# Performance work log

Hardware: AMD Instinct MI355X
Metric: run time of the kernel (lower is better)

## Reference

```python
import jax, jax.numpy as jnp
import numpy as np

B, IN_CH, OUT_CH = 4, 64, 128
N_HIGH, N_LOW = 163842, 40962
GROUPS, EPS, SLOPE = 4, 1e-5, 0.2


def setup_inputs() -> dict:
    key = jax.random.key(0)
    ks = jax.random.split(key, 6)
    x = jax.random.normal(ks[0], (B, IN_CH, N_HIGH), jnp.float32)
    pool_neigh = jax.random.randint(ks[1], (N_LOW * 7,), 0, N_HIGH, dtype=jnp.int32)
    conv_neigh = jax.random.randint(ks[2], (N_LOW * 7,), 0, N_LOW, dtype=jnp.int32)
    W1 = jax.random.normal(ks[3], (OUT_CH, 7 * IN_CH), jnp.float32) / np.float32(np.sqrt(7 * IN_CH))
    b1 = jnp.zeros((OUT_CH,), jnp.float32)
    W2 = jax.random.normal(ks[4], (OUT_CH, 7 * OUT_CH), jnp.float32) / np.float32(np.sqrt(7 * OUT_CH))
    b2 = jnp.zeros((OUT_CH,), jnp.float32)
    return dict(x=x, pool_neigh=pool_neigh, conv_neigh=conv_neigh,
                W1=W1, b1=b1, gn1_w=jnp.ones((OUT_CH,), jnp.float32), gn1_b=jnp.zeros((OUT_CH,), jnp.float32),
                W2=W2, b2=b2, gn2_w=jnp.ones((OUT_CH,), jnp.float32), gn2_b=jnp.zeros((OUT_CH,), jnp.float32))


def _mean_pool(x, pool_neigh):
    # x: (B, C, N_high); pool_neigh: (N_low*7,) -> (B, C, N_low)
    g = x[:, :, pool_neigh].reshape(x.shape[0], x.shape[1], -1, 7)
    return g.mean(axis=-1)


def _onering_conv(x, neigh, W, b):
    # x: (B, C, N); neigh: (N*7,); W: (O, 7*C). Torch Linear over gathered
    # (N*7, C).view(N, 7*C): neighbor-major, channel-minor concatenation.
    Bb, C, N = x.shape
    feat = x[:, :, neigh].reshape(Bb, C, N, 7)            # (B, C, N, 7)
    feat = jnp.transpose(feat, (0, 2, 3, 1)).reshape(Bb, N, 7 * C)  # (B, N, 7C)
    out = jnp.einsum('bnf,of->bno', feat, W) + b          # (B, N, O)
    return jnp.transpose(out, (0, 2, 1))                  # (B, O, N)


def _group_norm(x, w, b):
    # x: (B, C, N), normalize per (group, sample) over (C//G, N)
    Bb, C, N = x.shape
    xg = x.reshape(Bb, GROUPS, C // GROUPS, N)
    mu = xg.mean(axis=(2, 3), keepdims=True)
    var = ((xg - mu) ** 2).mean(axis=(2, 3), keepdims=True)
    xn = ((xg - mu) * jax.lax.rsqrt(var + EPS)).reshape(Bb, C, N)
    return xn * w[None, :, None] + b[None, :, None]


def _leaky_relu(x):
    return jnp.where(x >= 0, x, SLOPE * x)


def reference(x, pool_neigh, conv_neigh, W1, b1, gn1_w, gn1_b, W2, b2, gn2_w, gn2_b):
    h = _mean_pool(x, pool_neigh)
    h = _leaky_relu(_group_norm(_onering_conv(h, conv_neigh, W1, b1), gn1_w, gn1_b))
    h = _leaky_relu(_group_norm(_onering_conv(h, conv_neigh, W2, b2), gn2_w, gn2_b))
    return h
```

## Files before the change

kernel.cpp:

```cpp
#include <hip/hip_runtime.h>

#define B_SZ 4
#define IN_CH 64
#define OUT_CH 128
#define NHI 163842
#define NLO 40962
#define EPS_GN 1e-5f
#define SLOPE 0.2f

typedef __attribute__((ext_vector_type(8))) short short8;
typedef __attribute__((ext_vector_type(16))) float f32x16;

__device__ inline ushort f2bf(float f) {
    union { float f; unsigned u; } v; v.f = f;
    unsigned r = v.u + 0x7FFF + ((v.u >> 16) & 1);
    return (ushort)(r >> 16);
}
__device__ inline float bf2f(ushort h) {
    union { unsigned u; float f; } v; v.u = ((unsigned)h) << 16;
    return v.f;
}

__global__ void k_transpose_x(const float* __restrict__ x, ushort* __restrict__ xT) {
    __shared__ float t[64][65];
    const int b   = blockIdx.y;
    const int n0  = blockIdx.x * 64;
    const int tid = threadIdx.x;
    const int nq  = tid & 15;
    const int c0  = tid >> 4;
    const bool full = (n0 + 64) <= NHI;
    if (full) {
#pragma unroll
        for (int r = 0; r < 4; ++r) {
            int c = c0 + r * 16;
            float4 v = *(const float4*)&x[((long)b * IN_CH + c) * NHI + n0 + nq * 4];
            t[c][nq * 4 + 0] = v.x; t[c][nq * 4 + 1] = v.y;
            t[c][nq * 4 + 2] = v.z; t[c][nq * 4 + 3] = v.w;
        }
    } else {
        for (int r = 0; r < 4; ++r) {
            int c = c0 + r * 16;
            for (int e = 0; e < 4; ++e) {
                int n = n0 + nq * 4 + e;
                t[c][nq * 4 + e] = (n < NHI) ? x[((long)b * IN_CH + c) * NHI + n] : 0.f;
            }
        }
    }
    __syncthreads();
    const int n  = tid >> 2;
    const int cc = (tid & 3) * 16;
    if (n0 + n < NHI) {
        short8 o0, o1;
#pragma unroll
        for (int e = 0; e < 8; ++e) {
            o0[e] = (short)f2bf(t[cc + e][n]);
            o1[e] = (short)f2bf(t[cc + 8 + e][n]);
        }
        ushort* p = &xT[((long)b * NHI + n0 + n) * 64 + cc];
        *(short8*)p = o0;
        *(short8*)(p + 8) = o1;
    }
}

__global__ void k_prep_w(const float* __restrict__ W, ushort* __restrict__ Wb, int K) {
    int i = blockIdx.x * 256 + threadIdx.x;
    if (i >= K * 128) return;
    int k = i / 128, o = i % 128;
    int step = k >> 6, kk = k & 63, kg = kk >> 3, e = kk & 7;
    Wb[(((long)(step * 8 + kg) * 128 + o) * 8) + e] = f2bf(W[(long)o * K + k]);
}

__global__ void k_pool(const ushort* __restrict__ xT, const int* __restrict__ pn,
                       ushort* __restrict__ h1) {
    long t = (long)blockIdx.x * 256 + threadIdx.x;
    const long total = (long)B_SZ * NLO * 8;
    if (t >= total) return;
    int  cq = (int)(t & 7);
    long bn = t >> 3;
    int  n  = (int)(bn % NLO);
    int  b  = (int)(bn / NLO);
    float acc[8] = {};
#pragma unroll
    for (int j = 0; j < 7; ++j) {
        int idx = pn[n * 7 + j];
        short8 v = *(const short8*)&xT[((long)b * NHI + idx) * 64 + cq * 8];
#pragma unroll
        for (int e = 0; e < 8; ++e) acc[e] += bf2f((ushort)v[e]);
    }
    short8 o;
#pragma unroll
    for (int e = 0; e < 8; ++e) o[e] = (short)f2bf(acc[e] * (1.f / 7.f));
    *(short8*)&h1[bn * 64 + cq * 8] = o;
}

template <int CIN>
__global__ __launch_bounds__(512, 4)
void k_conv_mfma(const ushort* __restrict__ src, const int* __restrict__ nbr,
                 const ushort* __restrict__ Wb, const float* __restrict__ bias,
                 ushort* __restrict__ out, float* __restrict__ part) {
    constexpr int K = 7 * CIN;
    constexpr int NSTEP = K / 64;
    __shared__ ushort Asm[2][8 * 128 * 8];
    __shared__ ushort Bsm[2][8 * 128 * 8];
    __shared__ float  red[8][4];

    const int b    = blockIdx.y;
    const int n0   = blockIdx.x * 128;
    const int tid  = threadIdx.x;
    const int lane = tid & 63;
    const int wave = tid >> 6;
    const int wr   = wave >> 1, wc = wave & 1;

    const int s_nn = tid >> 2;
    const int s_kq = tid & 3;
    int nrow = n0 + s_nn; if (nrow >= NLO) nrow = NLO - 1;
    const int* nbr_row = &nbr[nrow * 7];

    f32x16 acc0 = {}, acc1 = {};
    const long srcb = (long)b * NLO * CIN;

    const int arow  = wr * 32 + (lane & 31);
    const int bcol0 = wc * 64 + (lane & 31);
    const int khalf = lane >> 5;

    short8 a0, a1, w0, w1;
    {
        int j = 0, cbase = 0;
        const ushort* sp = &src[srcb + (long)nbr_row[j] * CIN + cbase + s_kq * 8];
        a0 = *(const short8*)sp;
        a1 = *(const short8*)(sp + 32);
        const ushort* wp = &Wb[tid * 16];
        w0 = *(const short8*)wp;
        w1 = *(const short8*)(wp + 8);
    }

    for (int step = 0; step < NSTEP; ++step) {
        const int cur = step & 1;
        *(short8*)&Asm[cur][(s_kq * 128 + s_nn) * 8]       = a0;
        *(short8*)&Asm[cur][((s_kq + 4) * 128 + s_nn) * 8] = a1;
        *(short8*)&Bsm[cur][tid * 16]     = w0;
        *(short8*)&Bsm[cur][tid * 16 + 8] = w1;
        __syncthreads();
        if (step + 1 < NSTEP) {
            int s = step + 1, j, cbase;
            if (CIN == 64) { j = s; cbase = 0; }
            else           { j = s >> 1; cbase = (s & 1) * 64; }
            const ushort* sp = &src[srcb + (long)nbr_row[j] * CIN + cbase + s_kq * 8];
            a0 = *(const short8*)sp;
            a1 = *(const short8*)(sp + 32);
            const ushort* wp = &Wb[(long)s * 8192 + tid * 16];
            w0 = *(const short8*)wp;
            w1 = *(const short8*)(wp + 8);
        }
#pragma unroll
        for (int kh = 0; kh < 4; ++kh) {
            int kg = 2 * kh + khalf;
            short8 af  = *(const short8*)&Asm[cur][(kg * 128 + arow) * 8];
            short8 bf0 = *(const short8*)&Bsm[cur][(kg * 128 + bcol0) * 8];
            short8 bf1 = *(const short8*)&Bsm[cur][(kg * 128 + bcol0 + 32) * 8];
            acc0 = __builtin_amdgcn_mfma_f32_32x32x16_bf16(af, bf0, acc0, 0, 0, 0);
            acc1 = __builtin_amdgcn_mfma_f32_32x32x16_bf16(af, bf1, acc1, 0, 0, 0);
        }
    }

    const float bias0 = bias[wc * 64 + (lane & 31)];
    const float bias1 = bias[wc * 64 + 32 + (lane & 31)];
    float s0 = 0.f, q0 = 0.f, s1 = 0.f, q1 = 0.f;
#pragma unroll
    for (int r = 0; r < 16; ++r) {
        int rrow = (r & 3) + 8 * (r >> 2) + 4 * khalf + wr * 32;
        int n = n0 + rrow;
        float v0 = acc0[r] + bias0;
        float v1 = acc1[r] + bias1;
        if (n < NLO) {
            long o = ((long)b * NLO + n) * 128 + wc * 64 + (lane & 31);
            out[o]      = f2bf(v0);
            out[o + 32] = f2bf(v1);
            s0 += v0; q0 += v0 * v0;
            s1 += v1; q1 += v1 * v1;
        }
    }
#pragma unroll
    for (int off = 32; off > 0; off >>= 1) {
        s0 += __shfl_down(s0, off); q0 += __shfl_down(q0, off);
        s1 += __shfl_down(s1, off); q1 += __shfl_down(q1, off);
    }
    if (lane == 0) { red[wave][0] = s0; red[wave][1] = q0; red[wave][2] = s1; red[wave][3] = q1; }
    __syncthreads();
    if (tid < 8) {
        int g = tid >> 1, isq = tid & 1;
        int wcg = g >> 1, ct = g & 1;
        float v = 0.f;
#pragma unroll
        for (int w = 0; w < 4; ++w) v += red[w * 2 + wcg][ct * 2 + isq];
        part[(((long)b * gridDim.x + blockIdx.x) * 4 + g) * 2 + isq] = v;
    }
}

__global__ void k_finalize(const float* __restrict__ part, int nblk,
                           const float* __restrict__ w, const float* __restrict__ bb,
                           float* __restrict__ scale, float* __restrict__ shift) {
    const int b = blockIdx.x >> 2, g = blockIdx.x & 3;
    const int tid = threadIdx.x;
    float s = 0.f, ss = 0.f;
    for (int k = tid; k < nblk; k += 256) {
        s  += part[(((long)b * nblk + k) * 4 + g) * 2 + 0];
        ss += part[(((long)b * nblk + k) * 4 + g) * 2 + 1];
    }
#pragma unroll
    for (int off = 32; off > 0; off >>= 1) {
        s += __shfl_down(s, off); ss += __shfl_down(ss, off);
    }
    __shared__ float red[8];
    __shared__ float fin[2];
    const int wave = tid >> 6, lane = tid & 63;
    if (lane == 0) { red[wave * 2] = s; red[wave * 2 + 1] = ss; }
    __syncthreads();
    if (tid == 0) {
        float as = red[0] + red[2] + red[4] + red[6];
        float aq = red[1] + red[3] + red[5] + red[7];
        const float cnt = 32.f * NLO;
        float mu  = as / cnt;
        float var = aq / cnt - mu * mu;
        fin[0] = mu; fin[1] = rsqrtf(var + EPS_GN);
    }
    __syncthreads();
    if (tid < 32) {
        int c = g * 32 + tid;
        float sc = fin[1] * w[c];
        scale[b * 128 + c] = sc;
        shift[b * 128 + c] = bb[c] - fin[0] * sc;
    }
}

__global__ void k_gnapply(const ushort* __restrict__ y, const float* __restrict__ sc,
                          const float* __restrict__ sh, ushort* __restrict__ yp) {
    long t = (long)blockIdx.x * 256 + threadIdx.x;
    const long total = (long)B_SZ * NLO * 16;
    if (t >= total) return;
    int  c8 = (int)(t & 15);
    long bn = t >> 4;
    int  b  = (int)(bn / NLO);
    short8 v = *(const short8*)&y[bn * 128 + c8 * 8];
    short8 o;
#pragma unroll
    for (int e = 0; e < 8; ++e) {
        int c = c8 * 8 + e;
        float f = bf2f((ushort)v[e]) * sc[b * 128 + c] + sh[b * 128 + c];
        f = fmaxf(f, SLOPE * f);
        o[e] = (short)f2bf(f);
    }
    *(short8*)&yp[bn * 128 + c8 * 8] = o;
}

__global__ void k_output(const ushort* __restrict__ y2, const float* __restrict__ scale,
                         const float* __restrict__ shift, float* __restrict__ out) {
    __shared__ float t[32][129];
    const int b   = blockIdx.y;
    const int n0  = blockIdx.x * 32;
    const int tid = threadIdx.x;
    const float* scb = &scale[b * 128];
    const float* shb = &shift[b * 128];
    const int c8 = (tid & 15) * 8;
#pragma unroll
    for (int r = 0; r < 2; ++r) {
        int nn = (tid >> 4) + r * 16;
        int n  = n0 + nn;
        if (n < NLO) {
            short8 v = *(const short8*)&y2[((long)b * NLO + n) * 128 + c8];
#pragma unroll
            for (int e = 0; e < 8; ++e) {
                int c = c8 + e;
                float f = bf2f((ushort)v[e]) * scb[c] + shb[c];
                t[nn][c] = fmaxf(f, SLOPE * f);
            }
        } else {
#pragma unroll
            for (int e = 0; e < 8; ++e) t[nn][c8 + e] = 0.f;
        }
    }
    __syncthreads();
    const int n4 = (tid & 7) * 4;
    const bool full = (n0 + 32) <= NLO;
#pragma unroll
    for (int r = 0; r < 4; ++r) {
        int c = (tid >> 3) + r * 32;
        long o = ((long)b * 128 + c) * NLO + n0 + n4;
        if (full) {
            float2 v0 = make_float2(t[n4][c], t[n4 + 1][c]);
            float2 v1 = make_float2(t[n4 + 2][c], t[n4 + 3][c]);
            *(float2*)&out[o]     = v0;
            *(float2*)&out[o + 2] = v1;
        } else {
            for (int e = 0; e < 4; ++e)
                if (n0 + n4 + e < NLO) out[o + e] = t[n4 + e][c];
        }
    }
}

extern "C" void kernel_launch(void* const* d_in, const int* in_sizes, int n_in,
                              void* d_out, int out_size, void* d_ws, size_t ws_size,
                              hipStream_t stream) {
    const float* x   = (const float*)d_in[0];
    const int*   pn  = (const int*)d_in[1];
    const int*   cn  = (const int*)d_in[2];
    const float* W1  = (const float*)d_in[3];
    const float* b1  = (const float*)d_in[4];
    const float* g1w = (const float*)d_in[5];
    const float* g1b = (const float*)d_in[6];
    const float* W2  = (const float*)d_in[7];
    const float* b2  = (const float*)d_in[8];
    const float* g2w = (const float*)d_in[9];
    const float* g2b = (const float*)d_in[10];
    float* out = (float*)d_out;
    char*  base = (char*)d_ws;

    ushort* xT  = (ushort*)(base + 0);
    ushort* y1  = (ushort*)(base + 0);
    ushort* y1p = (ushort*)(base + 44000000);
    ushort* h1  = (ushort*)(base + 88000000);
    ushort* y2  = (ushort*)(base + 110000000);
    ushort* wb1 = (ushort*)(base + 152000000);
    ushort* wb2 = (ushort*)(base + 152200000);
    float*  p1  = (float*)(base + 152500000);
    float*  p2  = (float*)(base + 152600000);
    float*  sc1 = (float*)(base + 152700000);
    float*  sh1 = sc1 + 512;
    float*  sc2 = (float*)(base + 152710000);
    float*  sh2 = sc2 + 512;

    const int NBLK = (NLO + 127) / 128;

    k_transpose_x<<<dim3((NHI + 63) / 64, B_SZ), 256, 0, stream>>>(x, xT);
    k_prep_w<<<(448 * 128 + 255) / 256, 256, 0, stream>>>(W1, wb1, 448);
    k_prep_w<<<(896 * 128 + 255) / 256, 256, 0, stream>>>(W2, wb2, 896);
    k_pool<<<(int)(((long)B_SZ * NLO * 8 + 255) / 256), 256, 0, stream>>>(xT, pn, h1);
    k_conv_mfma<64><<<dim3(NBLK, B_SZ), 512, 0, stream>>>(h1, cn, wb1, b1, y1, p1);
    k_finalize<<<16, 256, 0, stream>>>(p1, NBLK, g1w, g1b, sc1, sh1);
    k_gnapply<<<(int)(((long)B_SZ * NLO * 16 + 255) / 256), 256, 0, stream>>>(y1, sc1, sh1, y1p);
    k_conv_mfma<128><<<dim3(NBLK, B_SZ), 512, 0, stream>>>(y1p, cn, wb2, b2, y2, p2);
    k_finalize<<<16, 256, 0, stream>>>(p2, NBLK, g2w, g2b, sc2, sh2);
    k_output<<<dim3((NLO + 31) / 32, B_SZ), 256, 0, stream>>>(y2, sc2, sh2, out);
}
```

Baseline: 248.0 us.

## Restructure conv MFMA kernel: register-resident A gathers, async LDS weight loads, larger tiles

Rewrites the gather-conv MFMA kernel. The gathered activation rows now go straight from global memory into registers in the MFMA operand layout, so A no longer passes through shared memory. Weights are copied into a double-buffered LDS tile with global_load_lds. Each block now covers 256 rows with 4 waves, and each wave computes a 64x128 tile, which raises per-wave reuse of the B fragments from LDS. The aim is to cut LDS traffic and barrier cost per MFMA, at the price of more registers per wave (8 accumulators plus a double set of A fragments) and fewer blocks in the grid.

```diff
diff --git a/kernel.cpp b/kernel.cpp
--- a/kernel.cpp
+++ b/kernel.cpp
@@ -19,6 +19,12 @@
 __device__ inline float bf2f(ushort h) {
     union { unsigned u; float f; } v; v.u = ((unsigned)h) << 16;
     return v.f;
+}
+
+__device__ inline void glds16(const ushort* g, ushort* l) {
+    typedef __attribute__((address_space(1))) const void gv;
+    typedef __attribute__((address_space(3))) void lv;
+    __builtin_amdgcn_global_load_lds((gv*)g, (lv*)l, 16, 0, 0);
 }
 
 __global__ void k_transpose_x(const float* __restrict__ x, ushort* __restrict__ xT) {
@@ -94,105 +100,131 @@
 }
 
 template <int CIN>
-__global__ __launch_bounds__(512, 4)
+__global__ __launch_bounds__(256, 2)
 void k_conv_mfma(const ushort* __restrict__ src, const int* __restrict__ nbr,
                  const ushort* __restrict__ Wb, const float* __restrict__ bias,
                  ushort* __restrict__ out, float* __restrict__ part) {
-    constexpr int K = 7 * CIN;
-    constexpr int NSTEP = K / 64;
-    __shared__ ushort Asm[2][8 * 128 * 8];
-    __shared__ ushort Bsm[2][8 * 128 * 8];
-    __shared__ float  red[8][4];
-
-    const int b    = blockIdx.y;
-    const int n0   = blockIdx.x * 128;
-    const int tid  = threadIdx.x;
-    const int lane = tid & 63;
-    const int wave = tid >> 6;
-    const int wr   = wave >> 1, wc = wave & 1;
-
-    const int s_nn = tid >> 2;
-    const int s_kq = tid & 3;
-    int nrow = n0 + s_nn; if (nrow >= NLO) nrow = NLO - 1;
-    const int* nbr_row = &nbr[nrow * 7];
-
-    f32x16 acc0 = {}, acc1 = {};
+    constexpr int NSTEP = 7 * CIN / 64;
+    __shared__ ushort Bsm[2][8192];
+    __shared__ float  red[4][4][2];
+
+    const int b     = blockIdx.y;
+    const int n0    = blockIdx.x * 256;
+    const int tid   = threadIdx.x;
+    const int lane  = tid & 63;
+    const int wid   = tid >> 6;
+    const int l31   = lane & 31;
+    const int khalf = lane >> 5;
+
+    const int rr0 = min(n0 + wid * 64 + l31, NLO - 1);
+    const int rr1 = min(n0 + wid * 64 + 32 + l31, NLO - 1);
+    int nb0[7], nb1[7];
+#pragma unroll
+    for (int j = 0; j < 7; ++j) {
+        nb0[j] = nbr[rr0 * 7 + j];
+        nb1[j] = nbr[rr1 * 7 + j];
+    }
+
     const long srcb = (long)b * NLO * CIN;
-
-    const int arow  = wr * 32 + (lane & 31);
-    const int bcol0 = wc * 64 + (lane & 31);
-    const int khalf = lane >> 5;
-
-    short8 a0, a1, w0, w1;
+    const int  koff = khalf * 8;
+
+    f32x16 acc[2][4] = {};
+    short8 a[2][4], an[2][4];
+
+#pragma unroll
+    for (int i = 0; i < 4; ++i) {
+        int off = (wid * 4 + i) * 512;
+        glds16(&Wb[off + lane * 8], &Bsm[0][off]);
+    }
     {
-        int j = 0, cbase = 0;
-        const ushort* sp = &src[srcb + (long)nbr_row[j] * CIN + cbase + s_kq * 8];
-        a0 = *(const short8*)sp;
-        a1 = *(const short8*)(sp + 32);
-        const ushort* wp = &Wb[tid * 16];
-        w0 = *(const short8*)wp;
-        w1 = *(const short8*)(wp + 8);
-    }
-
+        const ushort* s0 = &src[srcb + (long)nb0[0] * CIN + koff];
+        const ushort* s1 = &src[srcb + (long)nb1[0] * CIN + koff];
+#pragma unroll
+        for (int kh = 0; kh < 4; ++kh) {
+            a[0][kh] = *(const short8*)(s0 + kh * 16);
+            a[1][kh] = *(const short8*)(s1 + kh * 16);
+        }
+    }
+
+#pragma unroll
     for (int step = 0; step < NSTEP; ++step) {
         const int cur = step & 1;
-        *(short8*)&Asm[cur][(s_kq * 128 + s_nn) * 8]       = a0;
-        *(short8*)&Asm[cur][((s_kq + 4) * 128 + s_nn) * 8] = a1;
-        *(short8*)&Bsm[cur][tid * 16]     = w0;
-        *(short8*)&Bsm[cur][tid * 16 + 8] = w1;
         __syncthreads();
         if (step + 1 < NSTEP) {
-            int s = step + 1, j, cbase;
-            if (CIN == 64) { j = s; cbase = 0; }
-            else           { j = s >> 1; cbase = (s & 1) * 64; }
-            const ushort* sp = &src[srcb + (long)nbr_row[j] * CIN + cbase + s_kq * 8];
-            a0 = *(const short8*)sp;
-            a1 = *(const short8*)(sp + 32);
-            const ushort* wp = &Wb[(long)s * 8192 + tid * 16];
-            w0 = *(const short8*)wp;
-            w1 = *(const short8*)(wp + 8);
+#pragma unroll
+            for (int i = 0; i < 4; ++i) {
+                int off = (wid * 4 + i) * 512;
+                glds16(&Wb[(long)(step + 1) * 8192 + off + lane * 8], &Bsm[cur ^ 1][off]);
+            }
+            const int j2 = (CIN == 64) ? (step + 1) : ((step + 1) >> 1);
+            const int cb2 = (CIN == 64) ? 0 : (((step + 1) & 1) * 64);
+            const ushort* s0 = &src[srcb + (long)nb0[j2] * CIN + cb2 + koff];
+            const ushort* s1 = &src[srcb + (long)nb1[j2] * CIN + cb2 + koff];
+#pragma unroll
+            for (int kh = 0; kh < 4; ++kh) {
+                an[0][kh] = *(const short8*)(s0 + kh * 16);
+                an[1][kh] = *(const short8*)(s1 + kh * 16);
+            }
         }
 #pragma unroll
         for (int kh = 0; kh < 4; ++kh) {
-            int kg = 2 * kh + khalf;
-            short8 af  = *(const short8*)&Asm[cur][(kg * 128 + arow) * 8];
-            short8 bf0 = *(const short8*)&Bsm[cur][(kg * 128 + bcol0) * 8];
-            short8 bf1 = *(const short8*)&Bsm[cur][(kg * 128 + bcol0 + 32) * 8];
-            acc0 = __builtin_amdgcn_mfma_f32_32x32x16_bf16(af, bf0, acc0, 0, 0, 0);
-            acc1 = __builtin_amdgcn_mfma_f32_32x32x16_bf16(af, bf1, acc1, 0, 0, 0);
-        }
-    }
-
-    const float bias0 = bias[wc * 64 + (lane & 31)];
-    const float bias1 = bias[wc * 64 + 32 + (lane & 31)];
-    float s0 = 0.f, q0 = 0.f, s1 = 0.f, q1 = 0.f;
-#pragma unroll
-    for (int r = 0; r < 16; ++r) {
-        int rrow = (r & 3) + 8 * (r >> 2) + 4 * khalf + wr * 32;
-        int n = n0 + rrow;
-        float v0 = acc0[r] + bias0;
-        float v1 = acc1[r] + bias1;
-        if (n < NLO) {
-            long o = ((long)b * NLO + n) * 128 + wc * 64 + (lane & 31);
-            out[o]      = f2bf(v0);
-            out[o + 32] = f2bf(v1);
-            s0 += v0; q0 += v0 * v0;
-            s1 += v1; q1 += v1 * v1;
-        }
-    }
-#pragma unroll
-    for (int off = 32; off > 0; off >>= 1) {
-        s0 += __shfl_down(s0, off); q0 += __shfl_down(q0, off);
-        s1 += __shfl_down(s1, off); q1 += __shfl_down(q1, off);
-    }
-    if (lane == 0) { red[wave][0] = s0; red[wave][1] = q0; red[wave][2] = s1; red[wave][3] = q1; }
+            const int kg = 2 * kh + khalf;
+            const ushort* bb = &Bsm[cur][(kg * 128 + l31) * 8];
+            short8 b0 = *(const short8*)(bb);
+            short8 b1 = *(const short8*)(bb + 32 * 8);
+            short8 b2 = *(const short8*)(bb + 64 * 8);
+            short8 b3 = *(const short8*)(bb + 96 * 8);
+            acc[0][0] = __builtin_amdgcn_mfma_f32_32x32x16_bf16(a[0][kh], b0, acc[0][0], 0, 0, 0);
+            acc[0][1] = __builtin_amdgcn_mfma_f32_32x32x16_bf16(a[0][kh], b1, acc[0][1], 0, 0, 0);
+            acc[0][2] = __builtin_amdgcn_mfma_f32_32x32x16_bf16(a[0][kh], b2, acc[0][2], 0, 0, 0);
+            acc[0][3] = __builtin_amdgcn_mfma_f32_32x32x16_bf16(a[0][kh], b3, acc[0][3], 0, 0, 0);
+            acc[1][0] = __builtin_amdgcn_mfma_f32_32x32x16_bf16(a[1][kh], b0, acc[1][0], 0, 0, 0);
+            acc[1][1] = __builtin_amdgcn_mfma_f32_32x32x16_bf16(a[1][kh], b1, acc[1][1], 0, 0, 0);
+            acc[1][2] = __builtin_amdgcn_mfma_f32_32x32x16_bf16(a[1][kh], b2, acc[1][2], 0, 0, 0);
+            acc[1][3] = __builtin_amdgcn_mfma_f32_32x32x16_bf16(a[1][kh], b3, acc[1][3], 0, 0, 0);
+        }
+        if (step + 1 < NSTEP) {
+#pragma unroll
+            for (int kh = 0; kh < 4; ++kh) {
+                a[0][kh] = an[0][kh];
+                a[1][kh] = an[1][kh];
+            }
+        }
+    }
+
+    float bia[4];
+#pragma unroll
+    for (int n = 0; n < 4; ++n) bia[n] = bias[n * 32 + l31];
+    float s[4] = {}, q[4] = {};
+#pragma unroll
+    for (int m = 0; m < 2; ++m)
+#pragma unroll
+        for (int n = 0; n < 4; ++n)
+#pragma unroll
+            for (int r = 0; r < 16; ++r) {
+                int crow = (r & 3) + 8 * (r >> 2) + 4 * khalf;
+                int row  = n0 + wid * 64 + m * 32 + crow;
+                float v  = acc[m][n][r] + bia[n];
+                if (row < NLO) {
+                    out[((long)b * NLO + row) * 128 + n * 32 + l31] = f2bf(v);
+                    s[n] += v; q[n] += v * v;
+                }
+            }
+#pragma unroll
+    for (int n = 0; n < 4; ++n)
+#pragma unroll
+        for (int off = 32; off > 0; off >>= 1) {
+            s[n] += __shfl_down(s[n], off);
+            q[n] += __shfl_down(q[n], off);
+        }
+    if (lane == 0) {
+#pragma unroll
+        for (int n = 0; n < 4; ++n) { red[wid][n][0] = s[n]; red[wid][n][1] = q[n]; }
+    }
     __syncthreads();
     if (tid < 8) {
         int g = tid >> 1, isq = tid & 1;
-        int wcg = g >> 1, ct = g & 1;
-        float v = 0.f;
-#pragma unroll
-        for (int w = 0; w < 4; ++w) v += red[w * 2 + wcg][ct * 2 + isq];
+        float v = red[0][g][isq] + red[1][g][isq] + red[2][g][isq] + red[3][g][isq];
         part[(((long)b * gridDim.x + blockIdx.x) * 4 + g) * 2 + isq] = v;
     }
 }
@@ -329,16 +361,16 @@
     float*  sc2 = (float*)(base + 152710000);
     float*  sh2 = sc2 + 512;
 
-    const int NBLK = (NLO + 127) / 128;
+    const int NBLK = (NLO + 255) / 256;
 
     k_transpose_x<<<dim3((NHI + 63) / 64, B_SZ), 256, 0, stream>>>(x, xT);
     k_prep_w<<<(448 * 128 + 255) / 256, 256, 0, stream>>>(W1, wb1, 448);
     k_prep_w<<<(896 * 128 + 255) / 256, 256, 0, stream>>>(W2, wb2, 896);
     k_pool<<<(int)(((long)B_SZ * NLO * 8 + 255) / 256), 256, 0, stream>>>(xT, pn, h1);
-    k_conv_mfma<64><<<dim3(NBLK, B_SZ), 512, 0, stream>>>(h1, cn, wb1, b1, y1, p1);
+    k_conv_mfma<64><<<dim3(NBLK, B_SZ), 256, 0, stream>>>(h1, cn, wb1, b1, y1, p1);
     k_finalize<<<16, 256, 0, stream>>>(p1, NBLK, g1w, g1b, sc1, sh1);
     k_gnapply<<<(int)(((long)B_SZ * NLO * 16 + 255) / 256), 256, 0, stream>>>(y1, sc1, sh1, y1p);
-    k_conv_mfma<128><<<dim3(NBLK, B_SZ), 512, 0, stream>>>(y1p, cn, wb2, b2, y2, p2);
+    k_conv_mfma<128><<<dim3(NBLK, B_SZ), 256, 0, stream>>>(y1p, cn, wb2, b2, y2, p2);
     k_finalize<<<16, 256, 0, stream>>>(p2, NBLK, g2w, g2b, sc2, sh2);
     k_output<<<dim3((NLO + 31) / 32, B_SZ), 256, 0, stream>>>(y2, sc2, sh2, out);
 }
```

Result: slower. 272.0 us (+9.7%).

## Fuse GroupNorm apply into second conv and stream weights via LDS DMA

Applied to the files above, without the earlier changes.

Removes the separate GroupNorm+LeakyReLU pass between the two convolutions by applying scale/shift and activation while staging gathered neighbour rows into shared memory in the second conv. Weights are now copied straight to LDS with global_load_lds, A tiles use an XOR-swizzled LDS layout to cut bank conflicts, and gathers are prefetched two steps ahead with neighbour indices held in registers. This saves a full read and write of the intermediate activation, at the cost of redoing the normalisation on every gathered row (7x redundant ALU work) and higher register pressure.

```diff
diff --git a/kernel.cpp b/kernel.cpp
--- a/kernel.cpp
+++ b/kernel.cpp
@@ -9,6 +9,7 @@
 #define SLOPE 0.2f
 
 typedef __attribute__((ext_vector_type(8))) short short8;
+typedef __attribute__((ext_vector_type(8))) float float8;
 typedef __attribute__((ext_vector_type(16))) float f32x16;
 
 __device__ inline ushort f2bf(float f) {
@@ -19,6 +20,12 @@
 __device__ inline float bf2f(ushort h) {
     union { unsigned u; float f; } v; v.u = ((unsigned)h) << 16;
     return v.f;
+}
+
+__device__ inline void glds16(const ushort* g, ushort* l) {
+    typedef __attribute__((address_space(1))) const void gv;
+    typedef __attribute__((address_space(3))) void lv;
+    __builtin_amdgcn_global_load_lds((gv*)g, (lv*)l, 16, 0, 0);
 }
 
 __global__ void k_transpose_x(const float* __restrict__ x, ushort* __restrict__ xT) {
@@ -93,78 +100,100 @@
     *(short8*)&h1[bn * 64 + cq * 8] = o;
 }
 
-template <int CIN>
+__device__ inline int aidx(int kg, int nn) {
+    return (kg * 128 + (nn ^ ((kg & 7) << 1))) * 8;
+}
+
+template <int CIN, bool FUSE>
 __global__ __launch_bounds__(512, 4)
 void k_conv_mfma(const ushort* __restrict__ src, const int* __restrict__ nbr,
                  const ushort* __restrict__ Wb, const float* __restrict__ bias,
+                 const float* __restrict__ gsc, const float* __restrict__ gsh,
                  ushort* __restrict__ out, float* __restrict__ part) {
-    constexpr int K = 7 * CIN;
-    constexpr int NSTEP = K / 64;
-    __shared__ ushort Asm[2][8 * 128 * 8];
-    __shared__ ushort Bsm[2][8 * 128 * 8];
-    __shared__ float  red[8][4];
-
-    const int b    = blockIdx.y;
-    const int n0   = blockIdx.x * 128;
-    const int tid  = threadIdx.x;
-    const int lane = tid & 63;
-    const int wave = tid >> 6;
-    const int wr   = wave >> 1, wc = wave & 1;
+    constexpr int NSTEP = 7 * CIN / 64;
+    __shared__ ushort Asm[2][8192];
+    __shared__ ushort Bsm[2][8192];
+    __shared__ float  red[8][2][2];
+
+    const int b     = blockIdx.y;
+    const int n0    = blockIdx.x * 128;
+    const int tid   = threadIdx.x;
+    const int lane  = tid & 63;
+    const int wave  = tid >> 6;
+    const int wr    = wave >> 1, wc = wave & 1;
+    const int l31   = lane & 31;
+    const int khalf = lane >> 5;
 
     const int s_nn = tid >> 2;
     const int s_kq = tid & 3;
-    int nrow = n0 + s_nn; if (nrow >= NLO) nrow = NLO - 1;
-    const int* nbr_row = &nbr[nrow * 7];
-
+    const int nrow = min(n0 + s_nn, NLO - 1);
+    int nb[7];
+#pragma unroll
+    for (int j = 0; j < 7; ++j) nb[j] = nbr[nrow * 7 + j];
+
+    const long srcb = (long)b * NLO * CIN;
     f32x16 acc0 = {}, acc1 = {};
-    const long srcb = (long)b * NLO * CIN;
-
-    const int arow  = wr * 32 + (lane & 31);
-    const int bcol0 = wc * 64 + (lane & 31);
-    const int khalf = lane >> 5;
-
-    short8 a0, a1, w0, w1;
-    {
-        int j = 0, cbase = 0;
-        const ushort* sp = &src[srcb + (long)nbr_row[j] * CIN + cbase + s_kq * 8];
-        a0 = *(const short8*)sp;
-        a1 = *(const short8*)(sp + 32);
-        const ushort* wp = &Wb[tid * 16];
-        w0 = *(const short8*)wp;
-        w1 = *(const short8*)(wp + 8);
-    }
-
-    for (int step = 0; step < NSTEP; ++step) {
-        const int cur = step & 1;
-        *(short8*)&Asm[cur][(s_kq * 128 + s_nn) * 8]       = a0;
-        *(short8*)&Asm[cur][((s_kq + 4) * 128 + s_nn) * 8] = a1;
-        *(short8*)&Bsm[cur][tid * 16]     = w0;
-        *(short8*)&Bsm[cur][tid * 16 + 8] = w1;
+    short8 a[2][2];
+
+    auto loadA = [&](int t, short8* dst) {
+        const int j  = (CIN == 64) ? t : (t >> 1);
+        const int cb = (CIN == 64) ? 0 : ((t & 1) * 64);
+        const ushort* p = &src[srcb + (long)nb[j] * CIN + cb + s_kq * 8];
+        dst[0] = *(const short8*)p;
+        dst[1] = *(const short8*)(p + 32);
+    };
+    auto writeA = [&](int buf, int t, short8* v) {
+        short8 w0 = v[0], w1 = v[1];
+        if (FUSE) {
+            const int cb = (t & 1) * 64;
+            float8 sc0 = *(const float8*)&gsc[b * 128 + cb + s_kq * 8];
+            float8 sh0 = *(const float8*)&gsh[b * 128 + cb + s_kq * 8];
+            float8 sc1 = *(const float8*)&gsc[b * 128 + cb + s_kq * 8 + 32];
+            float8 sh1 = *(const float8*)&gsh[b * 128 + cb + s_kq * 8 + 32];
+#pragma unroll
+            for (int e = 0; e < 8; ++e) {
+                float f0 = bf2f((ushort)w0[e]) * sc0[e] + sh0[e];
+                float f1 = bf2f((ushort)w1[e]) * sc1[e] + sh1[e];
+                w0[e] = (short)f2bf(fmaxf(f0, SLOPE * f0));
+                w1[e] = (short)f2bf(fmaxf(f1, SLOPE * f1));
+            }
+        }
+        *(short8*)&Asm[buf][aidx(s_kq,     s_nn)] = w0;
+        *(short8*)&Asm[buf][aidx(s_kq + 4, s_nn)] = w1;
+    };
+    auto gldsB = [&](int t, int buf) {
+        glds16(&Wb[(long)t * 8192 + tid * 8],        &Bsm[buf][tid * 8]);
+        glds16(&Wb[(long)t * 8192 + tid * 8 + 4096], &Bsm[buf][tid * 8 + 4096]);
+    };
+
+    gldsB(0, 0);
+    loadA(0, a[0]);
+    if (NSTEP > 1) loadA(1, a[1]);
+    writeA(0, 0, a[0]);
+    __syncthreads();
+
+#pragma unroll
+    for (int s = 0; s < NSTEP; ++s) {
+        const int cur = s & 1, nxt = cur ^ 1;
+        if (s + 1 < NSTEP) {
+            gldsB(s + 1, nxt);
+            writeA(nxt, s + 1, a[(s + 1) & 1]);
+        }
+        if (s + 2 < NSTEP) loadA(s + 2, a[s & 1]);
+#pragma unroll
+        for (int kh = 0; kh < 4; ++kh) {
+            const int kg = 2 * kh + khalf;
+            short8 A0 = *(const short8*)&Asm[cur][aidx(kg, wr * 32 + l31)];
+            short8 B0 = *(const short8*)&Bsm[cur][(kg * 128 + wc * 64 + l31) * 8];
+            short8 B1 = *(const short8*)&Bsm[cur][(kg * 128 + wc * 64 + 32 + l31) * 8];
+            acc0 = __builtin_amdgcn_mfma_f32_32x32x16_bf16(A0, B0, acc0, 0, 0, 0);
+            acc1 = __builtin_amdgcn_mfma_f32_32x32x16_bf16(A0, B1, acc1, 0, 0, 0);
+        }
         __syncthreads();
-        if (step + 1 < NSTEP) {
-            int s = step + 1, j, cbase;
-            if (CIN == 64) { j = s; cbase = 0; }
-            else           { j = s >> 1; cbase = (s & 1) * 64; }
-            const ushort* sp = &src[srcb + (long)nbr_row[j] * CIN + cbase + s_kq * 8];
-            a0 = *(const short8*)sp;
-            a1 = *(const short8*)(sp + 32);
-            const ushort* wp = &Wb[(long)s * 8192 + tid * 16];
-            w0 = *(const short8*)wp;
-            w1 = *(const short8*)(wp + 8);
-        }
-#pragma unroll
-        for (int kh = 0; kh < 4; ++kh) {
-            int kg = 2 * kh + khalf;
-            short8 af  = *(const short8*)&Asm[cur][(kg * 128 + arow) * 8];
-            short8 bf0 = *(const short8*)&Bsm[cur][(kg * 128 + bcol0) * 8];
-            short8 bf1 = *(const short8*)&Bsm[cur][(kg * 128 + bcol0 + 32) * 8];
-            acc0 = __builtin_amdgcn_mfma_f32_32x32x16_bf16(af, bf0, acc0, 0, 0, 0);
-            acc1 = __builtin_amdgcn_mfma_f32_32x32x16_bf16(af, bf1, acc1, 0, 0, 0);
-        }
-    }
-
-    const float bias0 = bias[wc * 64 + (lane & 31)];
-    const float bias1 = bias[wc * 64 + 32 + (lane & 31)];
+    }
+
+    const float bias0 = bias[wc * 64 + l31];
+    const float bias1 = bias[wc * 64 + 32 + l31];
     float s0 = 0.f, q0 = 0.f, s1 = 0.f, q1 = 0.f;
 #pragma unroll
     for (int r = 0; r < 16; ++r) {
@@ -173,7 +202,7 @@
         float v0 = acc0[r] + bias0;
         float v1 = acc1[r] + bias1;
         if (n < NLO) {
-            long o = ((long)b * NLO + n) * 128 + wc * 64 + (lane & 31);
+            long o = ((long)b * NLO + n) * 128 + wc * 64 + l31;
             out[o]      = f2bf(v0);
             out[o + 32] = f2bf(v1);
             s0 += v0; q0 += v0 * v0;
@@ -185,14 +214,15 @@
         s0 += __shfl_down(s0, off); q0 += __shfl_down(q0, off);
         s1 += __shfl_down(s1, off); q1 += __shfl_down(q1, off);
     }
-    if (lane == 0) { red[wave][0] = s0; red[wave][1] = q0; red[wave][2] = s1; red[wave][3] = q1; }
+    if (lane == 0) { red[wave][0][0] = s0; red[wave][0][1] = q0;
+                     red[wave][1][0] = s1; red[wave][1][1] = q1; }
     __syncthreads();
     if (tid < 8) {
         int g = tid >> 1, isq = tid & 1;
-        int wcg = g >> 1, ct = g & 1;
+        int gwc = g >> 1, gn = g & 1;
         float v = 0.f;
 #pragma unroll
-        for (int w = 0; w < 4; ++w) v += red[w * 2 + wcg][ct * 2 + isq];
+        for (int w = 0; w < 4; ++w) v += red[w * 2 + gwc][gn][isq];
         part[(((long)b * gridDim.x + blockIdx.x) * 4 + g) * 2 + isq] = v;
     }
 }
@@ -231,26 +261,6 @@
         scale[b * 128 + c] = sc;
         shift[b * 128 + c] = bb[c] - fin[0] * sc;
     }
-}
-
-__global__ void k_gnapply(const ushort* __restrict__ y, const float* __restrict__ sc,
-                          const float* __restrict__ sh, ushort* __restrict__ yp) {
-    long t = (long)blockIdx.x * 256 + threadIdx.x;
-    const long total = (long)B_SZ * NLO * 16;
-    if (t >= total) return;
-    int  c8 = (int)(t & 15);
-    long bn = t >> 4;
-    int  b  = (int)(bn / NLO);
-    short8 v = *(const short8*)&y[bn * 128 + c8 * 8];
-    short8 o;
-#pragma unroll
-    for (int e = 0; e < 8; ++e) {
-        int c = c8 * 8 + e;
-        float f = bf2f((ushort)v[e]) * sc[b * 128 + c] + sh[b * 128 + c];
-        f = fmaxf(f, SLOPE * f);
-        o[e] = (short)f2bf(f);
-    }
-    *(short8*)&yp[bn * 128 + c8 * 8] = o;
 }
 
 __global__ void k_output(const ushort* __restrict__ y2, const float* __restrict__ scale,
@@ -317,16 +327,15 @@
 
     ushort* xT  = (ushort*)(base + 0);
     ushort* y1  = (ushort*)(base + 0);
-    ushort* y1p = (ushort*)(base + 44000000);
     ushort* h1  = (ushort*)(base + 88000000);
     ushort* y2  = (ushort*)(base + 110000000);
     ushort* wb1 = (ushort*)(base + 152000000);
     ushort* wb2 = (ushort*)(base + 152200000);
-    float*  p1  = (float*)(base + 152500000);
-    float*  p2  = (float*)(base + 152600000);
+    float*  p1  = (float*)(base + 110000000);
+    float*  p2  = (float*)(base + 88000000);
     float*  sc1 = (float*)(base + 152700000);
     float*  sh1 = sc1 + 512;
-    float*  sc2 = (float*)(base + 152710000);
+    float*  sc2 = (float*)(base + 152720000);
     float*  sh2 = sc2 + 512;
 
     const int NBLK = (NLO + 127) / 128;
@@ -335,10 +344,11 @@
     k_prep_w<<<(448 * 128 + 255) / 256, 256, 0, stream>>>(W1, wb1, 448);
     k_prep_w<<<(896 * 128 + 255) / 256, 256, 0, stream>>>(W2, wb2, 896);
     k_pool<<<(int)(((long)B_SZ * NLO * 8 + 255) / 256), 256, 0, stream>>>(xT, pn, h1);
-    k_conv_mfma<64><<<dim3(NBLK, B_SZ), 512, 0, stream>>>(h1, cn, wb1, b1, y1, p1);
+    k_conv_mfma<64, false><<<dim3(NBLK, B_SZ), 512, 0, stream>>>(
+        h1, cn, wb1, b1, nullptr, nullptr, y1, p1);
     k_finalize<<<16, 256, 0, stream>>>(p1, NBLK, g1w, g1b, sc1, sh1);
-    k_gnapply<<<(int)(((long)B_SZ * NLO * 16 + 255) / 256), 256, 0, stream>>>(y1, sc1, sh1, y1p);
-    k_conv_mfma<128><<<dim3(NBLK, B_SZ), 512, 0, stream>>>(y1p, cn, wb2, b2, y2, p2);
+    k_conv_mfma<128, true><<<dim3(NBLK, B_SZ), 512, 0, stream>>>(
+        y1, cn, wb2, b2, sc1, sh1, y2, p2);
     k_finalize<<<16, 256, 0, stream>>>(p2, NBLK, g2w, g2b, sc2, sh2);
     k_output<<<dim3((NLO + 31) / 32, B_SZ), 256, 0, stream>>>(y2, sc2, sh2, out);
 }
```

New measurement: 264.1 us. 6.5% more time.
